# Optimization experiments

Hardware: AMD Instinct MI355X
Metric: run time of the kernel (lower is better)

Reference implementation:

```python
import jax, jax.numpy as jnp
import numpy as np

N = 100000
E = 3200000
F_IN = 512
H = 128
C = 40


def gcn_conv(x, edge_index, edge_weight, W, b):
    """PyG GCNConv: x' = D^-1/2 (A+I) D^-1/2 (x W) + b, symmetric norm with self-loops."""
    n = x.shape[0]
    x = x @ W  # [N, H]
    row, col = edge_index[0], edge_index[1]
    sl = jnp.arange(n)
    row_f = jnp.concatenate([row, sl])
    col_f = jnp.concatenate([col, sl])
    w_f = jnp.concatenate([edge_weight, jnp.ones((n,), x.dtype)])
    deg = jax.ops.segment_sum(w_f, col_f, num_segments=n)  # in-degree incl. self-loop
    dinv = jnp.where(deg > 0, jax.lax.rsqrt(deg), 0.0)
    norm = dinv[row_f] * w_f * dinv[col_f]  # [E+N]
    msg = x[row_f] * norm[:, None]          # gather + scale
    out = jax.ops.segment_sum(msg, col_f, num_segments=n)  # scatter-add to targets
    return out + b


def setup_inputs() -> dict:
    key = jax.random.key(0)
    ks = jax.random.split(key, 12)
    inp = {
        "x": jax.random.normal(ks[0], (N, F_IN), jnp.float32),
        "edge_index": jax.random.randint(ks[1], (2, E), 0, N, jnp.int64),
        "edge_weight": jax.random.uniform(ks[2], (E,), jnp.float32),
        # first_lin
        "W1": jax.random.normal(ks[3], (F_IN, H), jnp.float32) / np.sqrt(F_IN),
        "b1": jnp.zeros((H,), jnp.float32),
        # conv layers (num_layers=2)
        "Wc1": jax.random.normal(ks[4], (H, H), jnp.float32) / np.sqrt(H),
        "bc1": jnp.zeros((H,), jnp.float32),
        "Wc2": jax.random.normal(ks[5], (H, H), jnp.float32) / np.sqrt(H),
        "bc2": jnp.zeros((H,), jnp.float32),
        # lin2
        "W2": jax.random.normal(ks[6], (H, C), jnp.float32) / np.sqrt(H),
        "b2": jnp.zeros((C,), jnp.float32),
        # wide layer
        "Ww": jax.random.normal(ks[7], (F_IN, C), jnp.float32) / np.sqrt(F_IN),
        "bw": jnp.zeros((C,), jnp.float32),
        # attention layer (-> 2 logits per node)
        "Wa": jax.random.normal(ks[8], (F_IN, 2), jnp.float32) / np.sqrt(F_IN),
        "ba": jnp.zeros((2,), jnp.float32),
    }
    return inp


def reference(x, edge_index, edge_weight, W1, b1, Wc1, bc1, Wc2, bc2, W2, b2, Ww, bw, Wa, ba):
    # deep branch (res_type=0.0, eval mode: dropout = identity)
    h = jax.nn.relu(x @ W1 + b1)
    h = jax.nn.relu(gcn_conv(h, edge_index, edge_weight, Wc1, bc1))
    h = jax.nn.relu(gcn_conv(h, edge_index, edge_weight, Wc2, bc2))
    deep_x = h @ W2 + b2  # [N, C]
    # wide branch on raw features
    wide_x = x @ Ww + bw  # [N, C]
    # attention fusion: softmax over 2 branch logits per node
    attn = jax.nn.softmax(x @ Wa + ba, axis=-1)  # [N, 2]
    out = deep_x * attn[:, 0:1] + wide_x * attn[:, 1:2]
    return out
```

## Files before the change

kernel.cpp:

```cpp
#include <hip/hip_runtime.h>
#include <hip/hip_bf16.h>
#include <cstdint>

#define N_NODES 100000
#define N_EDGES 3200000

typedef __attribute__((ext_vector_type(8))) short short8;
typedef __attribute__((ext_vector_type(4))) float floatx4;

#define FXS 8388608.0f
#define EA 320
#define EPB 10000
#define NBKT 391

__device__ __forceinline__ unsigned short f2bf(float f) {
    unsigned u = __float_as_uint(f);
    u += 0x7fff + ((u >> 16) & 1);
    return (unsigned short)(u >> 16);
}
__device__ __forceinline__ float bf2f(unsigned short s) {
    return __uint_as_float(((unsigned)s) << 16);
}
__device__ __forceinline__ float bflo(unsigned u) {
    return __uint_as_float(u << 16);
}
__device__ __forceinline__ float bfhi(unsigned u) {
    return __uint_as_float(u & 0xffff0000u);
}
__device__ __forceinline__ unsigned pack_bf2(float a, float b) {
    union { __hip_bfloat162 h2; unsigned u; } cv;
    cv.h2 = __float22bfloat162_rn(make_float2(a, b));
    return cv.u;
}

__global__ void setup_misc(const float* __restrict__ W1, const float* __restrict__ b1,
                           const float* __restrict__ Ww, const float* __restrict__ bw,
                           const float* __restrict__ Wa, const float* __restrict__ ba,
                           const float* __restrict__ Wc1, const float* __restrict__ Wc2,
                           const float* __restrict__ W2,
                           unsigned short* __restrict__ WcatT, float* __restrict__ bcat,
                           unsigned short* __restrict__ Wc1T, unsigned short* __restrict__ Wc2T,
                           unsigned short* __restrict__ W2T) {
    int bid = blockIdx.x, tid = threadIdx.x;
    if (bid < 192) {
        int c = bid;
        for (int kk = tid; kk < 512; kk += 256) {
            float v;
            if (c < 128)      v = W1[kk * 128 + c];
            else if (c < 168) v = Ww[kk * 40 + (c - 128)];
            else if (c < 170) v = Wa[kk * 2 + (c - 168)];
            else              v = 0.f;
            WcatT[(size_t)c * 512 + kk] = f2bf(v);
        }
        if (tid == 0) {
            float b;
            if (c < 128)      b = b1[c];
            else if (c < 168) b = bw[c - 128];
            else if (c < 170) b = ba[c - 168];
            else              b = 0.f;
            bcat[c] = b;
        }
    } else if (bid < 320) {
        int c = bid - 192;
        if (tid < 128) Wc1T[(size_t)c * 128 + tid] = f2bf(Wc1[tid * 128 + c]);
        else { int k = tid - 128; Wc2T[(size_t)c * 128 + k] = f2bf(Wc2[k * 128 + c]); }
    } else {
        int c = bid - 320;
        if (tid < 128)
            W2T[(size_t)c * 128 + tid] = (c < 40) ? f2bf(W2[tid * 40 + c])
                                                  : (unsigned short)0;
    }
}

template <int EPI, int NT, int AF32>
__device__ __forceinline__ void gemm_body(
    int mblk, const void* __restrict__ Avoid, const unsigned short* __restrict__ BT,
    int M, int K,
    unsigned short* __restrict__ C0, float* __restrict__ C1, float* __restrict__ C2,
    const float* __restrict__ bias, const float* __restrict__ rowscale) {
    constexpr int NB = 32 * NT;
    __shared__ __align__(16) unsigned short Ast[64 * 40];
    __shared__ __align__(16) unsigned short Bst[NB * 40];

    int tid = threadIdx.x;
    int m0 = mblk * 64;
    int wave = tid >> 6, lane = tid & 63;
    int quad = lane >> 4, mi = lane & 15;
    int wm = (wave >> 1) * 32;
    int wn = (wave & 1) * (16 * NT);

    int srow = tid >> 2;
    int sk8 = (tid & 3) * 8;

    int arow = m0 + srow; if (arow >= M) arow = M - 1;

    floatx4 acc[2][NT] = {};

    for (int kc = 0; kc < K; kc += 32) {
        if (AF32) {
            const float* Af = (const float*)Avoid;
            const float4* ap = (const float4*)(Af + (size_t)arow * K + kc + sk8);
            float4 f0 = ap[0], f1 = ap[1];
            uint4 pk;
            pk.x = pack_bf2(f0.x, f0.y);
            pk.y = pack_bf2(f0.z, f0.w);
            pk.z = pack_bf2(f1.x, f1.y);
            pk.w = pack_bf2(f1.z, f1.w);
            *(uint4*)&Ast[srow * 40 + sk8] = pk;
        } else {
            const unsigned short* Ab = (const unsigned short*)Avoid;
            uint4 av = *(const uint4*)(Ab + (size_t)arow * K + kc + sk8);
            *(uint4*)&Ast[srow * 40 + sk8] = av;
        }
#pragma unroll
        for (int i = tid; i < NB * 4; i += 256) {
            int brow = i >> 2;
            int bk8 = (i & 3) * 8;
            uint4 bv = *(const uint4*)(BT + (size_t)brow * K + kc + bk8);
            *(uint4*)&Bst[brow * 40 + bk8] = bv;
        }
        __syncthreads();

        short8 a0 = *(const short8*)&Ast[(wm + mi) * 40 + quad * 8];
        short8 a1 = *(const short8*)&Ast[(wm + 16 + mi) * 40 + quad * 8];
#pragma unroll
        for (int nt = 0; nt < NT; ++nt) {
            short8 b = *(const short8*)&Bst[(wn + nt * 16 + mi) * 40 + quad * 8];
            acc[0][nt] = __builtin_amdgcn_mfma_f32_16x16x32_bf16(a0, b, acc[0][nt], 0, 0, 0);
            acc[1][nt] = __builtin_amdgcn_mfma_f32_16x16x32_bf16(a1, b, acc[1][nt], 0, 0, 0);
        }
        __syncthreads();
    }

#pragma unroll
    for (int mt = 0; mt < 2; ++mt) {
#pragma unroll
        for (int nt = 0; nt < NT; ++nt) {
            floatx4 v = acc[mt][nt];
            int gn = wn + nt * 16 + mi;
#pragma unroll
            for (int r = 0; r < 4; ++r) {
                int gm = m0 + wm + mt * 16 + quad * 4 + r;
                if (gm >= M) continue;
                float val = v[r];
                if (EPI == 0) {
                    C0[(size_t)gm * 128 + gn] = f2bf(rowscale[gm] * val);
                } else if (EPI == 1) {
                    val += bias[gn];
                    if (gn < 128)      C0[(size_t)gm * 128 + gn] = f2bf(fmaxf(val, 0.f));
                    else if (gn < 168) C1[(size_t)gm * 40 + (gn - 128)] = val;
                    else if (gn < 170) C2[(size_t)gm * 2 + (gn - 168)] = val;
                } else {
                    if (gn < 40) {
                        float l0 = rowscale[gm * 2], l1 = rowscale[gm * 2 + 1];
                        float mx = fmaxf(l0, l1);
                        float e0 = __expf(l0 - mx), e1 = __expf(l1 - mx);
                        float inv = 1.f / (e0 + e1);
                        C1[(size_t)gm * 40 + gn] =
                            (val + bias[gn]) * (e0 * inv) +
                            C2[(size_t)gm * 40 + gn] * (e1 * inv);
                    }
                }
            }
        }
    }
}

__global__ __launch_bounds__(256) void megaA(
    const float* __restrict__ x, const unsigned short* __restrict__ WcatT,
    unsigned short* __restrict__ h0, float* __restrict__ wide, float* __restrict__ attnL,
    const float* __restrict__ bcat, const int* __restrict__ ei,
    int* __restrict__ histA, int M, int e) {
    int bid = blockIdx.x;
    if (bid >= EA) {
        gemm_body<1, 6, 1>(bid - EA, x, WcatT, M, 512, h0, wide, attnL, bcat, nullptr);
        return;
    }
    __shared__ unsigned lh[NBKT];
    int tid = threadIdx.x;
    for (int i = tid; i < NBKT; i += 256) lh[i] = 0;
    __syncthreads();
    int base = bid * EPB, end = base + EPB; if (end > e) end = e;
    for (int i = base + tid; i < end; i += 256) {
        int d = ei[e + i];
        atomicAdd(&lh[d >> 8], 1u);
    }
    __syncthreads();
    for (int k = tid; k < NBKT; k += 256) histA[k * EA + bid] = (int)lh[k];
}

__global__ __launch_bounds__(256) void scatterA(
    const int* __restrict__ ei, const float* __restrict__ ew,
    const int* __restrict__ offA, uint2* __restrict__ cs, int e) {
    int bid = blockIdx.x, tid = threadIdx.x;
    __shared__ unsigned lh[NBKT];
    __shared__ int lo[NBKT];
    for (int i = tid; i < NBKT; i += 256) { lh[i] = 0; lo[i] = offA[i * EA + bid]; }
    __syncthreads();
    int base = bid * EPB, end = base + EPB; if (end > e) end = e;
    for (int i = base + tid; i < end; i += 256) {
        int d = ei[e + i];
        int r = ei[i];
        float w = ew[i];
        int k = d >> 8;
        unsigned lr = atomicAdd(&lh[k], 1u);
        cs[lo[k] + (int)lr] = make_uint2((unsigned)r | ((unsigned)(d & 255) << 24),
                                         __float_as_uint(w));
    }
}

__global__ __launch_bounds__(1024) void passB1(
    const uint2* __restrict__ cs, const int* __restrict__ offA,
    int* __restrict__ ptr, float* __restrict__ dinv, int n, int e) {
    int k = blockIdx.x, tid = threadIdx.x;
    __shared__ unsigned lc[256], lw[256];
    __shared__ int ls[256];
    if (tid < 256) { lc[tid] = 0; lw[tid] = 0; }
    __syncthreads();
    int start = offA[k * EA];
    int end = (k == NBKT - 1) ? e : offA[(k + 1) * EA];
    for (int i = start + tid; i < end; i += 1024) {
        uint2 u = cs[i];
        int dlow = u.x >> 24;
        unsigned fx = (unsigned)(__uint_as_float(u.y) * FXS);
        atomicAdd(&lc[dlow], 1u);
        atomicAdd(&lw[dlow], fx);
    }
    __syncthreads();
    int v = (tid < 256) ? (int)lc[tid] : 0;
    if (tid < 256) ls[tid] = v;
    __syncthreads();
    for (int off = 1; off < 256; off <<= 1) {
        int t = (tid < 256 && tid >= off) ? ls[tid - off] : 0;
        __syncthreads();
        if (tid < 256) ls[tid] += t;
        __syncthreads();
    }
    if (tid < 256) {
        int d = (k << 8) + tid;
        if (d < n) {
            ptr[d]  = start + ls[tid] - v;
            dinv[d] = rsqrtf(1.0f + (float)lw[tid] * (1.0f / FXS));
        }
    }
    if (k == NBKT - 1 && tid == 0) ptr[n] = e;
}

__global__ __launch_bounds__(256) void megaB(
    const unsigned short* __restrict__ h0, const unsigned short* __restrict__ Wc1T,
    unsigned short* __restrict__ tmpB, const float* __restrict__ dinv,
    const uint2* __restrict__ cs, const int* __restrict__ offA,
    const int* __restrict__ ptr, uint2* __restrict__ edges, int M, int n, int e) {
    int bid = blockIdx.x;
    if (bid >= NBKT) {
        gemm_body<0, 4, 0>(bid - NBKT, h0, Wc1T, M, 128, tmpB, nullptr, nullptr, nullptr, dinv);
        return;
    }
    int k = bid, tid = threadIdx.x;
    __shared__ unsigned lc[256];
    __shared__ int lp[256];
    { lc[tid] = 0; int d = (k << 8) + tid; lp[tid] = (d < n) ? ptr[d] : 0; }
    __syncthreads();
    int start = offA[k * EA];
    int end = (k == NBKT - 1) ? e : offA[(k + 1) * EA];
    for (int i = start + tid; i < end; i += 256) {
        uint2 u = cs[i];
        int dlow = u.x >> 24;
        unsigned src = u.x & 0x00FFFFFFu;
        unsigned lr = atomicAdd(&lc[dlow], 1u);
        edges[lp[dlow] + (int)lr] = make_uint2(src, u.y);
    }
}

__global__ __launch_bounds__(256) void gemm_conv(
    const unsigned short* __restrict__ A, const unsigned short* __restrict__ BT,
    unsigned short* __restrict__ C0, const float* __restrict__ rowscale, int M) {
    gemm_body<0, 4, 0>(blockIdx.x, A, BT, M, 128, C0, nullptr, nullptr, nullptr, rowscale);
}

__global__ __launch_bounds__(256) void gemm_final(
    const unsigned short* __restrict__ A, const unsigned short* __restrict__ W2T,
    float* __restrict__ out, float* __restrict__ wide,
    const float* __restrict__ attnL, const float* __restrict__ b2, int M) {
    gemm_body<2, 2, 0>(blockIdx.x, A, W2T, M, 128, nullptr, out, wide, b2, attnL);
}

__global__ void scan1(const int* __restrict__ in, int* __restrict__ out,
                      int* __restrict__ bsum, int n) {
    __shared__ int s[1024];
    int tid = threadIdx.x;
    int i = blockIdx.x * 1024 + tid;
    int v = (i < n) ? in[i] : 0;
    s[tid] = v;
    __syncthreads();
    for (int off = 1; off < 1024; off <<= 1) {
        int t = (tid >= off) ? s[tid - off] : 0;
        __syncthreads();
        s[tid] += t;
        __syncthreads();
    }
    if (i < n) out[i] = s[tid] - v;
    if (tid == 1023) bsum[blockIdx.x] = s[1023];
}

__global__ void scan_bsums(int* bsum, int nb) {
    __shared__ int s[1024];
    int tid = threadIdx.x;
    int v = (tid < nb) ? bsum[tid] : 0;
    s[tid] = v;
    __syncthreads();
    for (int off = 1; off < 1024; off <<= 1) {
        int t = (tid >= off) ? s[tid - off] : 0;
        __syncthreads();
        s[tid] += t;
        __syncthreads();
    }
    if (tid < nb) bsum[tid] = s[tid] - v;
}

__global__ void scan_add(int* __restrict__ out, const int* __restrict__ bsum,
                         int n, int tailv) {
    int i = blockIdx.x * 1024 + threadIdx.x;
    if (i < n) out[i] += bsum[blockIdx.x];
    if (i == 0 && tailv >= 0) out[n] = tailv;
}

__global__ __launch_bounds__(256) void propagate(
    const unsigned int* __restrict__ tmp2,
    unsigned int* __restrict__ out2,
    const float* __restrict__ bias, const float* __restrict__ dinv,
    const int* __restrict__ ptr, const uint2* __restrict__ edges, int n) {
    int wave = threadIdx.x >> 6, lane = threadIdx.x & 63;
    int d = blockIdx.x * 4 + wave;
    if (d >= n) return;

    unsigned u = tmp2[(size_t)d * 64 + lane];
    float acc0 = bflo(u);
    float acc1 = bfhi(u);

    int p = ptr[d], p1 = ptr[d + 1];
    for (; p + 16 <= p1; p += 16) {
        uint2 q[16];
#pragma unroll
        for (int j = 0; j < 16; ++j) q[j] = edges[p + j];
        unsigned rv[16];
#pragma unroll
        for (int j = 0; j < 16; ++j) rv[j] = tmp2[(size_t)q[j].x * 64 + lane];
#pragma unroll
        for (int j = 0; j < 16; ++j) {
            float w = __uint_as_float(q[j].y);
            acc0 += w * bflo(rv[j]); acc1 += w * bfhi(rv[j]);
        }
    }
    for (; p + 4 <= p1; p += 4) {
        uint2 q[4];
#pragma unroll
        for (int j = 0; j < 4; ++j) q[j] = edges[p + j];
        unsigned rv[4];
#pragma unroll
        for (int j = 0; j < 4; ++j) rv[j] = tmp2[(size_t)q[j].x * 64 + lane];
#pragma unroll
        for (int j = 0; j < 4; ++j) {
            float w = __uint_as_float(q[j].y);
            acc0 += w * bflo(rv[j]); acc1 += w * bfhi(rv[j]);
        }
    }
    for (; p < p1; ++p) {
        uint2 q = edges[p];
        unsigned a = tmp2[(size_t)q.x * 64 + lane];
        float w = __uint_as_float(q.y);
        acc0 += w * bflo(a); acc1 += w * bfhi(a);
    }
    float di = dinv[d];
    float v0 = fmaxf(di * acc0 + bias[2 * lane], 0.f);
    float v1 = fmaxf(di * acc1 + bias[2 * lane + 1], 0.f);
    out2[(size_t)d * 64 + lane] = (unsigned)f2bf(v0) | ((unsigned)f2bf(v1) << 16);
}

extern "C" void kernel_launch(void* const* d_in, const int* in_sizes, int n_in,
                              void* d_out, int out_size, void* d_ws, size_t ws_size,
                              hipStream_t stream) {
    (void)in_sizes; (void)n_in; (void)out_size; (void)ws_size;
    const float* x   = (const float*)d_in[0];
    const int*   ei  = (const int*)d_in[1];
    const float* ew  = (const float*)d_in[2];
    const float* W1  = (const float*)d_in[3];
    const float* b1  = (const float*)d_in[4];
    const float* Wc1 = (const float*)d_in[5];
    const float* bc1 = (const float*)d_in[6];
    const float* Wc2 = (const float*)d_in[7];
    const float* bc2 = (const float*)d_in[8];
    const float* W2  = (const float*)d_in[9];
    const float* b2  = (const float*)d_in[10];
    const float* Ww  = (const float*)d_in[11];
    const float* bw  = (const float*)d_in[12];
    const float* Wa  = (const float*)d_in[13];
    const float* ba  = (const float*)d_in[14];
    float* out = (float*)d_out;

    const int N = N_NODES, E = N_EDGES;
    char* ws = (char*)d_ws;
    size_t off = 0;
    auto alloc = [&](size_t bytes) -> void* {
        void* p = ws + off;
        off = (off + bytes + 255) & ~(size_t)255;
        return p;
    };
    unsigned short* bufA = (unsigned short*)alloc((size_t)N * 128 * 2);
    unsigned short* bufB = (unsigned short*)alloc((size_t)N * 128 * 2);
    float* wide  = (float*)alloc((size_t)N * 40 * 4);
    float* attnL = (float*)alloc((size_t)N * 2 * 4);
    float* dinv  = (float*)alloc((size_t)N * 4);
    int*   histA = (int*)alloc((size_t)NBKT * EA * 4);
    uint2* cs    = (uint2*)alloc((size_t)E * 8);
    int*   ptr   = (int*)alloc((size_t)(N + 1) * 4);
    int*   bsum  = (int*)alloc(1024 * 4);
    uint2* edges = (uint2*)alloc((size_t)E * 8);
    unsigned short* WcatT = (unsigned short*)alloc((size_t)192 * 512 * 2);
    unsigned short* Wc1T  = (unsigned short*)alloc((size_t)128 * 128 * 2);
    unsigned short* Wc2T  = (unsigned short*)alloc((size_t)128 * 128 * 2);
    unsigned short* W2T   = (unsigned short*)alloc((size_t)64 * 128 * 2);
    float* bcat  = (float*)alloc(192 * 4);

    const int MB = (N + 63) / 64;
    const int NHA = NBKT * EA;

    setup_misc<<<384, 256, 0, stream>>>(W1, b1, Ww, bw, Wa, ba, Wc1, Wc2, W2,
                                        WcatT, bcat, Wc1T, Wc2T, W2T);

    megaA<<<EA + MB, 256, 0, stream>>>(x, WcatT, bufA, wide, attnL, bcat,
                                       ei, histA, N, E);

    int nbA = (NHA + 1023) / 1024;
    scan1<<<nbA, 1024, 0, stream>>>(histA, histA, bsum, NHA);
    scan_bsums<<<1, 1024, 0, stream>>>(bsum, nbA);
    scan_add<<<nbA, 1024, 0, stream>>>(histA, bsum, NHA, -1);

    scatterA<<<EA, 256, 0, stream>>>(ei, ew, histA, cs, E);

    passB1<<<NBKT, 1024, 0, stream>>>(cs, histA, ptr, dinv, N, E);

    megaB<<<NBKT + MB, 256, 0, stream>>>(bufA, Wc1T, bufB, dinv,
                                         cs, histA, ptr, edges, N, N, E);
    propagate<<<(N + 3) / 4, 256, 0, stream>>>((const unsigned int*)bufB, (unsigned int*)bufA,
                                               bc1, dinv, ptr, edges, N);

    gemm_conv<<<MB, 256, 0, stream>>>(bufA, Wc2T, bufB, dinv, N);
    propagate<<<(N + 3) / 4, 256, 0, stream>>>((const unsigned int*)bufB, (unsigned int*)bufA,
                                               bc2, dinv, ptr, edges, N);

    gemm_final<<<MB, 256, 0, stream>>>(bufA, W2T, out, wide, attnL, b2, N);
}
```

Measured before the change: 738.7 us.

## Split fused histogram/GEMM kernel and hoist B-tile loads in GEMM loop

Splits the combined megaA kernel, which ran the edge histogram and the input GEMM as different block ranges of one launch, into two separate launches on the same stream. The GEMM body also precomputes row pointers and B-tile indices outside the k-loop, and issues all B global loads into registers before the A load and the shared-memory stores to give more memory-level parallelism. Splitting loses the concurrent overlap of the histogram and GEMM blocks and adds a launch. In exchange each kernel gets a simpler, more uniform code path and register allocation.

```diff
diff --git a/kernel.cpp b/kernel.cpp
--- a/kernel.cpp
+++ b/kernel.cpp
@@ -79,6 +79,7 @@
     unsigned short* __restrict__ C0, float* __restrict__ C1, float* __restrict__ C2,
     const float* __restrict__ bias, const float* __restrict__ rowscale) {
     constexpr int NB = 32 * NT;
+    constexpr int RB = NT / 2;
     __shared__ __align__(16) unsigned short Ast[64 * 40];
     __shared__ __align__(16) unsigned short Bst[NB * 40];
 
@@ -94,13 +95,26 @@
 
     int arow = m0 + srow; if (arow >= M) arow = M - 1;
 
+    const float* Afp = (const float*)Avoid + (size_t)arow * K + sk8;
+    const unsigned short* Abp = (const unsigned short*)Avoid + (size_t)arow * K + sk8;
+    int brow[RB], bk8[RB];
+#pragma unroll
+    for (int r = 0; r < RB; ++r) {
+        int i = tid + r * 256;
+        brow[r] = i >> 2;
+        bk8[r] = (i & 3) * 8;
+    }
+
     floatx4 acc[2][NT] = {};
 
     for (int kc = 0; kc < K; kc += 32) {
+        uint4 bvs[RB];
+#pragma unroll
+        for (int r = 0; r < RB; ++r)
+            bvs[r] = *(const uint4*)(BT + (size_t)brow[r] * K + kc + bk8[r]);
         if (AF32) {
-            const float* Af = (const float*)Avoid;
-            const float4* ap = (const float4*)(Af + (size_t)arow * K + kc + sk8);
-            float4 f0 = ap[0], f1 = ap[1];
+            float4 f0 = *(const float4*)(Afp + kc);
+            float4 f1 = *(const float4*)(Afp + kc + 4);
             uint4 pk;
             pk.x = pack_bf2(f0.x, f0.y);
             pk.y = pack_bf2(f0.z, f0.w);
@@ -108,17 +122,12 @@
             pk.w = pack_bf2(f1.z, f1.w);
             *(uint4*)&Ast[srow * 40 + sk8] = pk;
         } else {
-            const unsigned short* Ab = (const unsigned short*)Avoid;
-            uint4 av = *(const uint4*)(Ab + (size_t)arow * K + kc + sk8);
+            uint4 av = *(const uint4*)(Abp + kc);
             *(uint4*)&Ast[srow * 40 + sk8] = av;
         }
 #pragma unroll
-        for (int i = tid; i < NB * 4; i += 256) {
-            int brow = i >> 2;
-            int bk8 = (i & 3) * 8;
-            uint4 bv = *(const uint4*)(BT + (size_t)brow * K + kc + bk8);
-            *(uint4*)&Bst[brow * 40 + bk8] = bv;
-        }
+        for (int r = 0; r < RB; ++r)
+            *(uint4*)&Bst[brow[r] * 40 + bk8[r]] = bvs[r];
         __syncthreads();
 
         short8 a0 = *(const short8*)&Ast[(wm + mi) * 40 + quad * 8];
@@ -166,16 +175,9 @@
     }
 }
 
-__global__ __launch_bounds__(256) void megaA(
-    const float* __restrict__ x, const unsigned short* __restrict__ WcatT,
-    unsigned short* __restrict__ h0, float* __restrict__ wide, float* __restrict__ attnL,
-    const float* __restrict__ bcat, const int* __restrict__ ei,
-    int* __restrict__ histA, int M, int e) {
+__global__ __launch_bounds__(256) void hist_k(
+    const int* __restrict__ ei, int* __restrict__ histA, int e) {
     int bid = blockIdx.x;
-    if (bid >= EA) {
-        gemm_body<1, 6, 1>(bid - EA, x, WcatT, M, 512, h0, wide, attnL, bcat, nullptr);
-        return;
-    }
     __shared__ unsigned lh[NBKT];
     int tid = threadIdx.x;
     for (int i = tid; i < NBKT; i += 256) lh[i] = 0;
@@ -187,6 +189,13 @@
     }
     __syncthreads();
     for (int k = tid; k < NBKT; k += 256) histA[k * EA + bid] = (int)lh[k];
+}
+
+__global__ __launch_bounds__(256) void gemm_in(
+    const float* __restrict__ x, const unsigned short* __restrict__ WcatT,
+    unsigned short* __restrict__ h0, float* __restrict__ wide, float* __restrict__ attnL,
+    const float* __restrict__ bcat, int M) {
+    gemm_body<1, 6, 1>(blockIdx.x, x, WcatT, M, 512, h0, wide, attnL, bcat, nullptr);
 }
 
 __global__ __launch_bounds__(256) void scatterA(
@@ -428,8 +437,9 @@
     setup_misc<<<384, 256, 0, stream>>>(W1, b1, Ww, bw, Wa, ba, Wc1, Wc2, W2,
                                         WcatT, bcat, Wc1T, Wc2T, W2T);
 
-    megaA<<<EA + MB, 256, 0, stream>>>(x, WcatT, bufA, wide, attnL, bcat,
-                                       ei, histA, N, E);
+    hist_k<<<EA, 256, 0, stream>>>(ei, histA, E);
+
+    gemm_in<<<MB, 256, 0, stream>>>(x, WcatT, bufA, wide, attnL, bcat, N);
 
     int nbA = (NHA + 1023) / 1024;
     scan1<<<nbA, 1024, 0, stream>>>(histA, histA, bsum, NHA);
```

New measurement: 757.3 us. 2.5% more time.
